# Performance work log

Measured on AMD Instinct MI355X. Metric: run time of the kernel, lower is better.

The kernel has to match this reference:

```python
import jax, jax.numpy as jnp
import numpy as np

D = 1024
H = 16
K = D // H
B = 2
S = 2048

def setup_inputs() -> dict:
    key = jax.random.key(0)
    k1, k2, k3, k4, k5 = jax.random.split(key, 5)
    x = jax.random.normal(k1, (B, S, D), dtype=jnp.float32)
    # nn.Linear(d, 3d): weight [3d, d], bias [3d]
    Wqkv = jax.random.normal(k2, (3 * D, D), dtype=jnp.float32) / np.sqrt(D)
    bqkv = jax.random.normal(k3, (3 * D,), dtype=jnp.float32) * 0.01
    Wproj = jax.random.normal(k4, (D, D), dtype=jnp.float32) / np.sqrt(D)
    bproj = jax.random.normal(k5, (D,), dtype=jnp.float32) * 0.01
    return {"x": x, "Wqkv": Wqkv, "bqkv": bqkv, "Wproj": Wproj, "bproj": bproj}

def reference(x, Wqkv, bqkv, Wproj, bproj):
    Bsz, Slen, d = x.shape
    # fused QKV projection: [B,S,3d] -> [B,S,3,H,K] -> (3, B, H, S, K)
    qkv = (jnp.einsum('bsd,ed->bse', x, Wqkv) + bqkv).reshape(Bsz, Slen, 3, H, K)
    q, k, v = jnp.moveaxis(qkv, 2, 0).transpose(0, 1, 3, 2, 4)
    scale = 1.0 / jnp.sqrt(jnp.asarray(K, dtype=x.dtype))
    scores = jnp.einsum('bhqk,bhmk->bhqm', q, k) * scale  # [B,H,S,S]
    a = jax.nn.softmax(scores, axis=-1)
    # dropout is identity in eval mode
    o = jnp.einsum('bhqm,bhmk->bhqk', a, v)  # [B,H,S,K]
    o = o.transpose(0, 2, 1, 3).reshape(Bsz, Slen, d)
    return jnp.einsum('bsd,ed->bse', o, Wproj) + bproj
```

## Files before the change

kernel.cpp:

```cpp
#include <hip/hip_runtime.h>
#include <cstdint>

typedef unsigned short ushort_t;
typedef short short8 __attribute__((ext_vector_type(8)));
typedef float f32x4 __attribute__((ext_vector_type(4)));
typedef float float4v __attribute__((ext_vector_type(4)));
typedef unsigned int uint2v __attribute__((ext_vector_type(2)));
typedef unsigned int uint4v __attribute__((ext_vector_type(4)));

#define DDIM 1024
#define HH 16
#define HEADK 64
#define BB 2
#define SS 2048

#if __has_builtin(__builtin_amdgcn_exp2f)
#define EXP2F(x) __builtin_amdgcn_exp2f(x)
#else
#define EXP2F(x) exp2f(x)
#endif

__device__ __forceinline__ ushort_t f2bf(float f) {
  union { float f; uint32_t u; } c; c.f = f;
  uint32_t u = c.u;
  u += 0x7fffu + ((u >> 16) & 1u);
  return (ushort_t)(u >> 16);
}

__device__ __forceinline__ uint32_t pkbf_trunc(float a, float b) {
  union { float f; uint32_t u; } ca, cb;
  ca.f = a; cb.f = b;
  return __builtin_amdgcn_perm(cb.u, ca.u, 0x07060302);
}

__device__ __forceinline__ uint32_t pkbf_rne(float a, float b) {
  return (uint32_t)f2bf(a) | ((uint32_t)f2bf(b) << 16);
}

__device__ __forceinline__ float bfhi2f(uint32_t u) {
  union { uint32_t u; float f; } c; c.u = u & 0xffff0000u; return c.f;
}
__device__ __forceinline__ float bflo2f(uint32_t u) {
  union { uint32_t u; float f; } c; c.u = u << 16; return c.f;
}

__device__ __forceinline__ void glds16(const ushort_t* gp, ushort_t* lp) {
  __builtin_amdgcn_global_load_lds(
      (const __attribute__((address_space(1))) uint32_t*)gp,
      (__attribute__((address_space(3))) uint32_t*)lp, 16, 0, 0);
}

__global__ void cvt3_kernel(const float* __restrict__ s0, ushort_t* __restrict__ d0, int n0,
                            const float* __restrict__ s1, ushort_t* __restrict__ d1, int n1,
                            const float* __restrict__ s2, ushort_t* __restrict__ d2, int n2) {
  int i = blockIdx.x * blockDim.x + threadIdx.x;
  const float* src; ushort_t* dst; int k;
  if (i < n0) { src = s0; dst = d0; k = i; }
  else if (i < n0 + n1) { src = s1; dst = d1; k = i - n0; }
  else if (i < n0 + n1 + n2) { src = s2; dst = d2; k = i - n0 - n1; }
  else return;
  float4v v = ((const float4v*)src)[k];
  uint2v o; o[0] = pkbf_rne(v[0], v[1]); o[1] = pkbf_rne(v[2], v[3]);
  ((uint2v*)dst)[k] = o;
}

__global__ __launch_bounds__(256) void gemm_qkv128(
    const ushort_t* __restrict__ A, const ushort_t* __restrict__ Bm,
    const float* __restrict__ bias, ushort_t* __restrict__ Cbf) {
  constexpr int Kd = 1024;
  __shared__ ushort_t smem[128 * 64 * 2];
  ushort_t* As = smem;
  ushort_t* Bs = smem + 128 * 64;
  const int tid = threadIdx.x;
  const int wv = tid >> 6, lane = tid & 63;
  const int l15 = lane & 15, quad = lane >> 4;
  const int wm = wv >> 1, wn = wv & 1;
  const int tm0 = blockIdx.y * 128, tn0 = blockIdx.x * 128;

  f32x4 acc[4][4];
#pragma unroll
  for (int i = 0; i < 4; ++i)
#pragma unroll
    for (int j = 0; j < 4; ++j) acc[i][j] = (f32x4){0.f, 0.f, 0.f, 0.f};

  const int lrow = lane >> 3;
  const int gcb = (lane & 7) ^ lrow;

  for (int k0 = 0; k0 < Kd; k0 += 64) {
#pragma unroll
    for (int c = 0; c < 4; ++c) {
      int seg = wv * 4 + c;
      glds16(A + (size_t)(tm0 + seg * 8 + lrow) * Kd + k0 + gcb * 8,
             As + seg * 512);
    }
#pragma unroll
    for (int c = 0; c < 4; ++c) {
      int seg = wv * 4 + c;
      glds16(Bm + (size_t)(tn0 + seg * 8 + lrow) * Kd + k0 + gcb * 8,
             Bs + seg * 512);
    }
    __syncthreads();
#pragma unroll
    for (int kk = 0; kk < 64; kk += 32) {
      short8 af[4], bfr[4];
#pragma unroll
      for (int i = 0; i < 4; ++i) {
        int r = wm * 64 + i * 16 + l15;
        int cb = (kk >> 3) + quad;
        af[i] = *(const short8*)(As + r * 64 + ((cb ^ (l15 & 7)) << 3));
      }
#pragma unroll
      for (int j = 0; j < 4; ++j) {
        int r = wn * 64 + j * 16 + l15;
        int cb = (kk >> 3) + quad;
        bfr[j] = *(const short8*)(Bs + r * 64 + ((cb ^ (l15 & 7)) << 3));
      }
#pragma unroll
      for (int i = 0; i < 4; ++i)
#pragma unroll
        for (int j = 0; j < 4; ++j)
          acc[i][j] = __builtin_amdgcn_mfma_f32_16x16x32_bf16(
              af[i], bfr[j], acc[i][j], 0, 0, 0);
    }
    __syncthreads();
  }

  const int t = tn0 >> 10;
  if (t < 2) {
#pragma unroll
    for (int j = 0; j < 4; ++j) {
      int col = tn0 + wn * 64 + j * 16 + l15;
      float bv = bias[col];
      int hh = (col >> 6) & 15, kk2 = col & 63;
#pragma unroll
      for (int i = 0; i < 4; ++i) {
        int row0 = tm0 + wm * 64 + i * 16 + quad * 4;
#pragma unroll
        for (int r = 0; r < 4; ++r) {
          int row = row0 + r;
          int b = row >> 11, s = row & 2047;
          float v = acc[i][j][r] + bv;
          if (t == 0) v *= 0.18033688f;
          size_t base = (((size_t)t * BB + b) * HH + hh) * ((size_t)SS * HEADK);
          Cbf[base + (size_t)s * HEADK + kk2] = f2bf(v);
        }
      }
    }
  } else {
    __syncthreads();
#pragma unroll
    for (int j = 0; j < 4; ++j) {
      int c = wn * 64 + j * 16 + l15;
      float bv = bias[tn0 + c];
#pragma unroll
      for (int i = 0; i < 4; ++i) {
        int row0 = wm * 64 + i * 16 + quad * 4;
        uint2v dw;
        dw[0] = pkbf_rne(acc[i][j][0] + bv, acc[i][j][1] + bv);
        dw[1] = pkbf_rne(acc[i][j][2] + bv, acc[i][j][3] + bv);
        int rb = row0 >> 3;
        *(uint2v*)(&smem[c * 128 + (((rb ^ (c & 15)) << 3) | (row0 & 7))]) = dw;
      }
    }
    __syncthreads();
    const int rb2 = lane & 15;
    const int cg = lane >> 4;
#pragma unroll
    for (int it = 0; it < 8; ++it) {
      int c = wv * 32 + it * 4 + cg;
      short8 vv = *(const short8*)(&smem[c * 128 + ((rb2 ^ (c & 15)) << 3)]);
      int gcol = tn0 + c;
      int hh = (gcol >> 6) & 15, kk2 = gcol & 63;
      int grow = tm0 + rb2 * 8;
      int b = grow >> 11, s = grow & 2047;
      size_t base = (((size_t)2 * BB + b) * HH + hh) * ((size_t)SS * HEADK);
      *(short8*)(&Cbf[base + (size_t)kk2 * SS + s]) = vv;
    }
  }
}

__global__ __launch_bounds__(512, 2) void gemm_proj(
    const ushort_t* __restrict__ Op0, const ushort_t* __restrict__ Op1,
    const float* __restrict__ Lp, const ushort_t* __restrict__ Bm,
    const float* __restrict__ bias, float* __restrict__ Cout) {
  constexpr int Kd = 1024;
  constexpr size_t nsL = (size_t)BB * HH * SS;
  __shared__ ushort_t smem[32768];
  const int tid = threadIdx.x;
  const int wv = tid >> 6, lane = tid & 63;
  const int l15 = lane & 15, quad = lane >> 4;
  const int wm = wv >> 2, wn = wv & 3;
  const int tm0 = blockIdx.y * 128, tn0 = blockIdx.x * 128;
  const int lrow = lane >> 3, gcb = (lane & 7) ^ lrow;

  const int ar = tid >> 2, acg = tid & 3;
  const int grow = tm0 + ar;
  const int ab = grow >> 11, as_ = grow & 2047;

  f32x4 acc[4][2];
#pragma unroll
  for (int i = 0; i < 4; ++i)
#pragma unroll
    for (int j = 0; j < 2; ++j) acc[i][j] = (f32x4){0.f, 0.f, 0.f, 0.f};

  uint4v ra0, ra1, rb0, rb1;
  float rl0, rl1;

  auto readA = [&](int t) {
    size_t lo = (size_t)(ab * HH + t) * SS + as_;
    size_t po = lo * 64 + acg * 16;
    ra0 = *(const uint4v*)(Op0 + po);
    ra1 = *(const uint4v*)(Op0 + po + 8);
    rb0 = *(const uint4v*)(Op1 + po);
    rb1 = *(const uint4v*)(Op1 + po + 8);
    rl0 = Lp[lo];
    rl1 = Lp[nsL + lo];
  };
  auto writeA = [&](int p) {
    float inv = 1.0f / (rl0 + rl1);
    uint4v olo, ohi;
#pragma unroll
    for (int d = 0; d < 4; ++d) {
      olo[d] = pkbf_rne((bflo2f(ra0[d]) + bflo2f(rb0[d])) * inv,
                        (bfhi2f(ra0[d]) + bfhi2f(rb0[d])) * inv);
      ohi[d] = pkbf_rne((bflo2f(ra1[d]) + bflo2f(rb1[d])) * inv,
                        (bfhi2f(ra1[d]) + bfhi2f(rb1[d])) * inv);
    }
    ushort_t* As = smem + p * 16384;
    *(uint4v*)(&As[ar * 64 + (((acg * 2) ^ (ar & 7)) << 3)]) = olo;
    *(uint4v*)(&As[ar * 64 + (((acg * 2 + 1) ^ (ar & 7)) << 3)]) = ohi;
  };
  auto stageB = [&](int t, int p) {
    ushort_t* Bs = smem + p * 16384 + 8192;
#pragma unroll
    for (int c = 0; c < 2; ++c) {
      int seg = wv * 2 + c;
      glds16(Bm + (size_t)(tn0 + seg * 8 + lrow) * Kd + t * 64 + gcb * 8,
             Bs + seg * 512);
    }
  };

  readA(0);
  __builtin_amdgcn_sched_barrier(0);
  stageB(0, 0);
  __builtin_amdgcn_sched_barrier(0);
  asm volatile("s_waitcnt vmcnt(2)" ::: "memory");
  writeA(0);

  for (int t = 0; t < 16; ++t) {
    const int p = t & 1;
    asm volatile("s_waitcnt lgkmcnt(0)" ::: "memory");
    __builtin_amdgcn_s_barrier();
    __builtin_amdgcn_sched_barrier(0);
    if (t + 1 < 16) {
      readA(t + 1);
      __builtin_amdgcn_sched_barrier(0);
      stageB(t + 1, p ^ 1);
      __builtin_amdgcn_sched_barrier(0);
      asm volatile("s_waitcnt vmcnt(8)" ::: "memory");
    } else {
      asm volatile("s_waitcnt vmcnt(0)" ::: "memory");
    }
    __builtin_amdgcn_s_barrier();
    asm volatile("" ::: "memory");
    __builtin_amdgcn_sched_barrier(0);

    const ushort_t* As = smem + p * 16384;
    const ushort_t* Bs = As + 8192;
    short8 bfr[2][2], af[4][2];
#pragma unroll
    for (int j = 0; j < 2; ++j)
#pragma unroll
      for (int kc = 0; kc < 2; ++kc) {
        int n = wn * 32 + j * 16 + l15;
        bfr[j][kc] =
            *(const short8*)(Bs + n * 64 + (((kc * 4 + quad) ^ (l15 & 7)) << 3));
      }
#pragma unroll
    for (int mi = 0; mi < 4; ++mi)
#pragma unroll
      for (int kc = 0; kc < 2; ++kc) {
        int r = wm * 64 + mi * 16 + l15;
        af[mi][kc] =
            *(const short8*)(As + r * 64 + (((kc * 4 + quad) ^ (l15 & 7)) << 3));
      }
    __builtin_amdgcn_s_setprio(1);
#pragma unroll
    for (int kc = 0; kc < 2; ++kc)
#pragma unroll
      for (int mi = 0; mi < 4; ++mi)
#pragma unroll
        for (int j = 0; j < 2; ++j)
          acc[mi][j] = __builtin_amdgcn_mfma_f32_16x16x32_bf16(
              af[mi][kc], bfr[j][kc], acc[mi][j], 0, 0, 0);
    __builtin_amdgcn_s_setprio(0);

    if (t + 1 < 16) writeA(p ^ 1);
  }

#pragma unroll
  for (int j = 0; j < 2; ++j) {
    int col = tn0 + wn * 32 + j * 16 + l15;
    float bv = bias[col];
#pragma unroll
    for (int mi = 0; mi < 4; ++mi) {
      int row0 = tm0 + wm * 64 + mi * 16 + quad * 4;
#pragma unroll
      for (int r = 0; r < 4; ++r)
        Cout[(size_t)(row0 + r) * 1024 + col] = acc[mi][j][r] + bv;
    }
  }
}

template <int NSPLIT>
__global__ __launch_bounds__(256, 4) void attn_kernel(
    const ushort_t* __restrict__ qkv, ushort_t* __restrict__ O0,
    ushort_t* __restrict__ O1, float* __restrict__ Lp) {
  constexpr int NT = (SS / NSPLIT) / 32;
  __shared__ ushort_t Kt[3][32 * 64];
  __shared__ ushort_t Vt[3][64 * 32];
  __shared__ ushort_t Pw[4][2][32 * 32];

  const int lin = blockIdx.x + 16 * (blockIdx.y + 16 * blockIdx.z);
  const int xcd = lin & 7, ii = lin >> 3;
  const int qt = ii & 15;
  const int hz = (ii >> 4) * 8 + xcd;
  const int h = hz & 15;
  const int z = hz >> 4;
  const int b = z >> 1, ns = z & 1;
  const int tid = threadIdx.x;
  const int wv = tid >> 6, lane = tid & 63;
  const int l15 = lane & 15, quad = lane >> 4;

  const size_t hstride = (size_t)SS * HEADK;
  const ushort_t* Qg = qkv + ((size_t)(0 * BB + b) * HH + h) * hstride;
  const ushort_t* Kg = qkv + ((size_t)(1 * BB + b) * HH + h) * hstride;
  const ushort_t* Vg = qkv + ((size_t)(2 * BB + b) * HH + h) * hstride;
  ushort_t* Opp = ns ? O1 : O0;

  short8 qf[2][2];
#pragma unroll
  for (int mi = 0; mi < 2; ++mi)
#pragma unroll
    for (int kc = 0; kc < 2; ++kc)
      qf[mi][kc] = *(const short8*)(
          Qg + (size_t)(qt * 128 + wv * 32 + mi * 16 + l15) * 64 + kc * 32 +
          quad * 8);

  const short ONE = (short)0x3F80;
  short8 ones = {ONE, ONE, ONE, ONE, ONE, ONE, ONE, ONE};

  f32x4 oat[2][4];
  f32x4 loa[2];
#pragma unroll
  for (int mi = 0; mi < 2; ++mi) {
    loa[mi] = (f32x4){0.f, 0.f, 0.f, 0.f};
#pragma unroll
    for (int c = 0; c < 4; ++c) oat[mi][c] = (f32x4){0.f, 0.f, 0.f, 0.f};
  }

  const int lrow = lane >> 3, gcb = (lane & 7) ^ lrow;
  const int vfl = lane >> 2;
  const int vgb = (lane & 3) ^ ((vfl >> 1) & 3);

  const int pos0 = ns * (SS / NSPLIT);

  auto stage = [&](int jj, int db) {
    glds16(Kg + (size_t)(pos0 + jj * 32 + wv * 8 + lrow) * 64 + gcb * 8,
           &Kt[db][wv * 512]);
    glds16(Vg + (size_t)(wv * 16 + vfl) * SS + pos0 + jj * 32 + vgb * 8,
           &Vt[db][wv * 512]);
  };

  auto qk_phase = [&](int kb, int pb) {
    f32x4 st[2][2];
    __builtin_amdgcn_s_setprio(1);
#pragma unroll
    for (int cf = 0; cf < 2; ++cf) {
      int n = cf * 16 + l15;
      short8 kf0 = *(const short8*)(&Kt[kb][n * 64 + ((quad ^ (n & 7)) << 3)]);
      short8 kf1 =
          *(const short8*)(&Kt[kb][n * 64 + (((quad + 4) ^ (n & 7)) << 3)]);
#pragma unroll
      for (int mi = 0; mi < 2; ++mi) {
        f32x4 z2 = (f32x4){0.f, 0.f, 0.f, 0.f};
        z2 = __builtin_amdgcn_mfma_f32_16x16x32_bf16(kf0, qf[mi][0], z2, 0, 0, 0);
        z2 = __builtin_amdgcn_mfma_f32_16x16x32_bf16(kf1, qf[mi][1], z2, 0, 0, 0);
        st[mi][cf] = z2;
      }
    }
    __builtin_amdgcn_s_setprio(0);
#pragma unroll
    for (int mi = 0; mi < 2; ++mi)
#pragma unroll
      for (int cf = 0; cf < 2; ++cf) {
        float e0 = EXP2F(st[mi][cf][0]);
        float e1 = EXP2F(st[mi][cf][1]);
        float e2 = EXP2F(st[mi][cf][2]);
        float e3 = EXP2F(st[mi][cf][3]);
        uint2v dw;
        dw[0] = pkbf_trunc(e0, e1);
        dw[1] = pkbf_trunc(e2, e3);
        int row = mi * 16 + l15;
        int pbv = 2 * cf + (quad >> 1);
        int pbs = pbv ^ ((l15 >> 1) & 3);
        *(uint2v*)(&Pw[wv][pb][row * 32 + pbs * 8 + (quad & 1) * 4]) = dw;
      }
  };

  stage(0, 0);
  stage(1, 1);

  asm volatile("s_waitcnt vmcnt(2)" ::: "memory");
  __builtin_amdgcn_s_barrier();
  asm volatile("" ::: "memory");
  __builtin_amdgcn_sched_barrier(0);
  qk_phase(0, 0);

  int vb = 0;
  for (int j = 0; j < NT; ++j) {
    const int kb = (vb == 2) ? 0 : vb + 1;
    const int sb = (kb == 2) ? 0 : kb + 1;
    asm volatile("s_waitcnt vmcnt(0)" ::: "memory");
    __builtin_amdgcn_s_barrier();
    asm volatile("" ::: "memory");
    __builtin_amdgcn_sched_barrier(0);

    if (j + 2 < NT) stage(j + 2, sb);
    if (j + 1 < NT) qk_phase(kb, (j + 1) & 1);

    short8 pa[2];
#pragma unroll
    for (int mi = 0; mi < 2; ++mi) {
      int row = mi * 16 + l15;
      pa[mi] = *(const short8*)(&Pw[wv][j & 1][row * 32 +
                                              ((quad ^ ((l15 >> 1) & 3)) << 3)]);
    }
    __builtin_amdgcn_s_setprio(1);
#pragma unroll
    for (int cf = 0; cf < 4; ++cf) {
      short8 vf = *(const short8*)(&Vt[vb][(cf * 16 + l15) * 32 +
                                           ((quad ^ ((l15 >> 1) & 3)) << 3)]);
#pragma unroll
      for (int mi = 0; mi < 2; ++mi)
        oat[mi][cf] = __builtin_amdgcn_mfma_f32_16x16x32_bf16(
            vf, pa[mi], oat[mi][cf], 0, 0, 0);
    }
#pragma unroll
    for (int mi = 0; mi < 2; ++mi)
      loa[mi] = __builtin_amdgcn_mfma_f32_16x16x32_bf16(ones, pa[mi], loa[mi],
                                                        0, 0, 0);
    __builtin_amdgcn_s_setprio(0);

    vb = kb;
  }

  const size_t obase = ((size_t)b * HH + h) * SS * HEADK;
#pragma unroll
  for (int mi = 0; mi < 2; ++mi) {
#pragma unroll
    for (int cf = 0; cf < 4; ++cf) {
      uint2v dw;
      dw[0] = pkbf_rne(oat[mi][cf][0], oat[mi][cf][1]);
      dw[1] = pkbf_rne(oat[mi][cf][2], oat[mi][cf][3]);
      int cb = 2 * cf + (quad >> 1);
      int cbs = cb ^ (l15 & 7);
      *(uint2v*)(&Pw[wv][0][l15 * 64 + cbs * 8 + (quad & 1) * 4]) = dw;
    }
    const int r = lane >> 2;
#pragma unroll
    for (int pass = 0; pass < 2; ++pass) {
      int g = (lane & 3) + 4 * pass;
      short8 ov = *(const short8*)(&Pw[wv][0][r * 64 + ((g ^ (r & 7)) << 3)]);
      int qrow = qt * 128 + wv * 32 + mi * 16 + r;
      *(short8*)(&Opp[obase + (size_t)qrow * 64 + g * 8]) = ov;
    }
    if (quad == 0) {
      int qrow = qt * 128 + wv * 32 + mi * 16 + l15;
      Lp[((size_t)(ns * BB + b) * HH + h) * SS + qrow] = loa[mi][0];
    }
  }
}

extern "C" void kernel_launch(void* const* d_in, const int* in_sizes, int n_in,
                              void* d_out, int out_size, void* d_ws,
                              size_t ws_size, hipStream_t stream) {
  const float* x = (const float*)d_in[0];
  const float* Wqkv = (const float*)d_in[1];
  const float* bqkv = (const float*)d_in[2];
  const float* Wproj = (const float*)d_in[3];
  const float* bproj = (const float*)d_in[4];
  float* out = (float*)d_out;

  ushort_t* xb = (ushort_t*)d_ws;
  ushort_t* wqb = xb + (size_t)4096 * 1024;
  ushort_t* wpb = wqb + (size_t)3072 * 1024;
  ushort_t* qkvb = wpb + (size_t)1024 * 1024;
  ushort_t* Op1 = qkvb + (size_t)3 * BB * HH * SS * HEADK;
  ushort_t* Op0 = xb;
  float* Lp = (float*)wqb;

  const int n0 = 4096 * 1024 / 4, n1 = 3072 * 1024 / 4, n2 = 1024 * 1024 / 4;
  cvt3_kernel<<<(n0 + n1 + n2 + 255) / 256, 256, 0, stream>>>(
      x, xb, n0, Wqkv, wqb, n1, Wproj, wpb, n2);
  gemm_qkv128<<<dim3(3072 / 128, 4096 / 128), 256, 0, stream>>>(xb, wqb, bqkv,
                                                                qkvb);
  attn_kernel<2><<<dim3(16, 16, 4), 256, 0, stream>>>(qkvb, Op0, Op1, Lp);
  gemm_proj<<<dim3(1024 / 128, 4096 / 128), 512, 0, stream>>>(
      Op0, Op1, Lp, wpb, bproj, out);
}
```

Measured before the change: 193.6 us.

## Remap GEMM blocks for XCD locality and shrink projection tile to 128x64

Both GEMM kernels now remap their linear block index so consecutive blocks on the same XCD share row tiles, aiming to improve L2 reuse across the eight chiplets. The output-projection GEMM moves from 512-thread 128x128 tiles to 256-thread 128x64 tiles, doubling the grid. Each thread now loads two rows of the split attention partials and merges them. The smaller tile raises the block count and occupancy, but the merge of the A operand (partials and normalizers) is repeated across twice as many column blocks.

Result: no change. 191.8 us (-0.9%).

```diff
diff --git a/kernel.cpp b/kernel.cpp
--- a/kernel.cpp
+++ b/kernel.cpp
@@ -75,7 +75,12 @@
   const int wv = tid >> 6, lane = tid & 63;
   const int l15 = lane & 15, quad = lane >> 4;
   const int wm = wv >> 1, wn = wv & 1;
-  const int tm0 = blockIdx.y * 128, tn0 = blockIdx.x * 128;
+
+  const int lin = blockIdx.x + 24 * blockIdx.y;
+  const int xcd = lin & 7, g = lin >> 3;
+  const int by = xcd + 8 * (g & 3);
+  const int bx = g >> 2;
+  const int tm0 = by * 128, tn0 = bx * 128;
 
   f32x4 acc[4][4];
 #pragma unroll
@@ -179,23 +184,24 @@
   }
 }
 
-__global__ __launch_bounds__(512, 2) void gemm_proj(
+__global__ __launch_bounds__(256, 2) void gemm_proj(
     const ushort_t* __restrict__ Op0, const ushort_t* __restrict__ Op1,
     const float* __restrict__ Lp, const ushort_t* __restrict__ Bm,
     const float* __restrict__ bias, float* __restrict__ Cout) {
   constexpr int Kd = 1024;
   constexpr size_t nsL = (size_t)BB * HH * SS;
-  __shared__ ushort_t smem[32768];
+  __shared__ ushort_t smem[2 * 12288];
   const int tid = threadIdx.x;
   const int wv = tid >> 6, lane = tid & 63;
   const int l15 = lane & 15, quad = lane >> 4;
-  const int wm = wv >> 2, wn = wv & 3;
-  const int tm0 = blockIdx.y * 128, tn0 = blockIdx.x * 128;
+  const int wm = wv >> 1, wn = wv & 1;
   const int lrow = lane >> 3, gcb = (lane & 7) ^ lrow;
 
-  const int ar = tid >> 2, acg = tid & 3;
-  const int grow = tm0 + ar;
-  const int ab = grow >> 11, as_ = grow & 2047;
+  const int lin = blockIdx.x + 16 * blockIdx.y;
+  const int xcd = lin & 7, g = lin >> 3;
+  const int by = xcd + 8 * (g & 3);
+  const int bx = g >> 2;
+  const int tm0 = by * 128, tn0 = bx * 64;
 
   f32x4 acc[4][2];
 #pragma unroll
@@ -203,35 +209,47 @@
 #pragma unroll
     for (int j = 0; j < 2; ++j) acc[i][j] = (f32x4){0.f, 0.f, 0.f, 0.f};
 
-  uint4v ra0, ra1, rb0, rb1;
-  float rl0, rl1;
+  uint4v ra0[2], ra1[2], rb0[2], rb1[2];
+  float rl0[2], rl1[2];
 
   auto readA = [&](int t) {
-    size_t lo = (size_t)(ab * HH + t) * SS + as_;
-    size_t po = lo * 64 + acg * 16;
-    ra0 = *(const uint4v*)(Op0 + po);
-    ra1 = *(const uint4v*)(Op0 + po + 8);
-    rb0 = *(const uint4v*)(Op1 + po);
-    rb1 = *(const uint4v*)(Op1 + po + 8);
-    rl0 = Lp[lo];
-    rl1 = Lp[nsL + lo];
+#pragma unroll
+    for (int c = 0; c < 2; ++c) {
+      int u = tid + 256 * c;
+      int row = u >> 2, cg = u & 3;
+      int grow = tm0 + row;
+      int ab = grow >> 11, as_ = grow & 2047;
+      size_t lo = (size_t)(ab * HH + t) * SS + as_;
+      size_t po = lo * 64 + cg * 16;
+      ra0[c] = *(const uint4v*)(Op0 + po);
+      ra1[c] = *(const uint4v*)(Op0 + po + 8);
+      rb0[c] = *(const uint4v*)(Op1 + po);
+      rb1[c] = *(const uint4v*)(Op1 + po + 8);
+      rl0[c] = Lp[lo];
+      rl1[c] = Lp[nsL + lo];
+    }
   };
   auto writeA = [&](int p) {
-    float inv = 1.0f / (rl0 + rl1);
-    uint4v olo, ohi;
-#pragma unroll
-    for (int d = 0; d < 4; ++d) {
-      olo[d] = pkbf_rne((bflo2f(ra0[d]) + bflo2f(rb0[d])) * inv,
-                        (bfhi2f(ra0[d]) + bfhi2f(rb0[d])) * inv);
-      ohi[d] = pkbf_rne((bflo2f(ra1[d]) + bflo2f(rb1[d])) * inv,
-                        (bfhi2f(ra1[d]) + bfhi2f(rb1[d])) * inv);
-    }
-    ushort_t* As = smem + p * 16384;
-    *(uint4v*)(&As[ar * 64 + (((acg * 2) ^ (ar & 7)) << 3)]) = olo;
-    *(uint4v*)(&As[ar * 64 + (((acg * 2 + 1) ^ (ar & 7)) << 3)]) = ohi;
+    ushort_t* As = smem + p * 12288;
+#pragma unroll
+    for (int c = 0; c < 2; ++c) {
+      int u = tid + 256 * c;
+      int row = u >> 2, cg = u & 3;
+      float inv = 1.0f / (rl0[c] + rl1[c]);
+      uint4v olo, ohi;
+#pragma unroll
+      for (int d = 0; d < 4; ++d) {
+        olo[d] = pkbf_rne((bflo2f(ra0[c][d]) + bflo2f(rb0[c][d])) * inv,
+                          (bfhi2f(ra0[c][d]) + bfhi2f(rb0[c][d])) * inv);
+        ohi[d] = pkbf_rne((bflo2f(ra1[c][d]) + bflo2f(rb1[c][d])) * inv,
+                          (bfhi2f(ra1[c][d]) + bfhi2f(rb1[c][d])) * inv);
+      }
+      *(uint4v*)(&As[row * 64 + (((cg * 2) ^ (row & 7)) << 3)]) = olo;
+      *(uint4v*)(&As[row * 64 + (((cg * 2 + 1) ^ (row & 7)) << 3)]) = ohi;
+    }
   };
   auto stageB = [&](int t, int p) {
-    ushort_t* Bs = smem + p * 16384 + 8192;
+    ushort_t* Bs = smem + p * 12288 + 8192;
 #pragma unroll
     for (int c = 0; c < 2; ++c) {
       int seg = wv * 2 + c;
@@ -257,7 +275,7 @@
       __builtin_amdgcn_sched_barrier(0);
       stageB(t + 1, p ^ 1);
       __builtin_amdgcn_sched_barrier(0);
-      asm volatile("s_waitcnt vmcnt(8)" ::: "memory");
+      asm volatile("s_waitcnt vmcnt(14)" ::: "memory");
     } else {
       asm volatile("s_waitcnt vmcnt(0)" ::: "memory");
     }
@@ -265,7 +283,7 @@
     asm volatile("" ::: "memory");
     __builtin_amdgcn_sched_barrier(0);
 
-    const ushort_t* As = smem + p * 16384;
+    const ushort_t* As = smem + p * 12288;
     const ushort_t* Bs = As + 8192;
     short8 bfr[2][2], af[4][2];
 #pragma unroll
@@ -506,6 +524,6 @@
   gemm_qkv128<<<dim3(3072 / 128, 4096 / 128), 256, 0, stream>>>(xb, wqb, bqkv,
                                                                 qkvb);
   attn_kernel<2><<<dim3(16, 16, 4), 256, 0, stream>>>(qkvb, Op0, Op1, Lp);
-  gemm_proj<<<dim3(1024 / 128, 4096 / 128), 512, 0, stream>>>(
+  gemm_proj<<<dim3(1024 / 64, 4096 / 128), 256, 0, stream>>>(
       Op0, Op1, Lp, wpb, bproj, out);
 }
```
